# Kernel tuning notes

Measured on AMD Instinct MI355X. Metric: run time of the kernel, lower is better.

The kernel has to match this reference:

```python
import jax, jax.numpy as jnp
import numpy as np

NUM_CLASSES = 1000
NUM_NEIGHBOURS = 200
SIGMA = 10.0
GAUSS_CONST = 1.0 / (2.0 * SIGMA ** 2)


def setup_inputs() -> dict:
    key = jax.random.key(0)
    k1, k2, k3 = jax.random.split(key, 3)
    B, D, C = 512, 512, 100000
    features = jax.random.normal(k1, (B, D), dtype=jnp.float32)
    centres = jax.random.normal(k2, (C, D), dtype=jnp.float32)
    centre_labels = jax.random.randint(k3, (C,), 0, NUM_CLASSES)
    weight = jnp.zeros((C,), dtype=jnp.float32)
    return {"features": features, "centres": centres,
            "centre_labels": centre_labels, "weight": weight}


def _knn(features, centres, k):
    # squared euclidean distances [B, C] without materializing [B, C, D]
    f2 = jnp.sum(features * features, axis=1, keepdims=True)      # [B,1]
    c2 = jnp.sum(centres * centres, axis=1)                        # [C]
    d2 = f2 + c2[None, :] - 2.0 * features @ centres.T             # [B,C]
    _, idx = jax.lax.top_k(-d2, k)                                 # smallest k
    return idx                                                     # [B,k]


def reference(features, centres, centre_labels, weight):
    B = features.shape[0]
    K = NUM_NEIGHBOURS
    nbr = _knn(features, centres, K)                               # [B,K] int
    gathered = centres[nbr]                                        # [B,K,D]
    d2 = jnp.sum((features[:, None, :] - gathered) ** 2, axis=-1)  # [B,K]
    kernel_weights = jnp.exp(weight)                               # [C]
    d = jnp.exp(-d2 * GAUSS_CONST) * kernel_weights[nbr]           # [B,K]
    nbr_labels = centre_labels[nbr]                                # [B,K]
    rows = jnp.arange(B)[:, None]
    p = jnp.zeros((B, NUM_CLASSES), dtype=d.dtype).at[rows, nbr_labels].add(d)
    p = jnp.where(p == 0, 1e-10, p)
    p = p / jnp.sum(p, axis=1, keepdims=True)
    return jnp.log(p)
```

## Files before the change

### kernel.cpp

```cpp
#include <hip/hip_runtime.h>
#include <hip/hip_fp16.h>
#include <math.h>
#include <stdint.h>

#define D_DIM    512
#define NCLS     1000
#define KSEL     200
#define NBINS    1024
#define HREP     4
#define CAND_MAX 2048
#define GCONST   0.005
#define MARGIN   4.0f

typedef short s8v __attribute__((ext_vector_type(8)));
typedef float f4v __attribute__((ext_vector_type(4)));

#define GLOAD_LDS16(gp, lp) __builtin_amdgcn_global_load_lds( \
    (const __attribute__((address_space(1))) void*)(gp),      \
    (__attribute__((address_space(3))) void*)(lp), 16, 0, 0)

static __device__ __forceinline__ unsigned short f2bf(float x) {
    unsigned u = __float_as_uint(x);
    return (unsigned short)((u + 0x7FFFu + ((u >> 16) & 1u)) >> 16);
}

static __device__ __forceinline__ unsigned cvt_pk_bf16(float lo, float hi) {
    unsigned r;
    asm("v_cvt_pk_bf16_f32 %0, %1, %2" : "=v"(r) : "v"(lo), "v"(hi));
    return r;
}

__global__ __launch_bounds__(256)
void convertF(const float* __restrict__ F, unsigned short* __restrict__ Fb,
              float* __restrict__ f2)
{
    __shared__ float red[256];
    const int r = blockIdx.x, t = threadIdx.x;
    float2 v = *(const float2*)(F + (size_t)r * D_DIM + t * 2);
    ushort2 o; o.x = f2bf(v.x); o.y = f2bf(v.y);
    *(ushort2*)(Fb + (size_t)r * D_DIM + t * 2) = o;
    red[t] = v.x * v.x + v.y * v.y;
    __syncthreads();
    for (int off = 128; off > 0; off >>= 1) {
        if (t < off) red[t] += red[t + off];
        __syncthreads();
    }
    if (t == 0) f2[r] = red[0];
}

__global__ __launch_bounds__(512)
void mfma_gemm(const unsigned short* __restrict__ Fb,
               const float* __restrict__ C,
               const float* __restrict__ f2,
               __half* __restrict__ Dm, int N)
{
    __shared__ short smem[32 * 512 + 16 * 512];
    __shared__ float c2s[128];
    short* As = smem;
    short* Bs = smem + 32 * 512;
    const int t    = threadIdx.x;
    const int lane = t & 63;
    const int w    = t >> 6;
    const int wm   = w >> 1, wn = w & 1;
    const int m0   = blockIdx.x * 256;
    const int n0   = blockIdx.y * 128;
    const int lrow = lane >> 3;
    const int oct  = (lane & 7) ^ lrow;
    const int quad = lane >> 4;
    const int col  = lane & 15;

    f4v acc[4][4];
#pragma unroll
    for (int i = 0; i < 4; ++i)
#pragma unroll
        for (int j = 0; j < 4; ++j) acc[i][j] = (f4v){0.f, 0.f, 0.f, 0.f};

    float  c2part[2] = {0.f, 0.f};
    float4 ra[2], rb[2];

#pragma unroll
    for (int cc = 0; cc < 2; ++cc) {
        int row = (w * 2 + cc) * 8 + lrow;
        int rg  = n0 + row; rg = rg < N ? rg : N - 1;
        const float* gp = C + (size_t)rg * D_DIM + oct * 8;
        ra[cc] = *(const float4*)gp;
        rb[cc] = *(const float4*)(gp + 4);
    }

    for (int k0 = 0; k0 < D_DIM; k0 += 64) {
        __syncthreads();
#pragma unroll
        for (int cc = 0; cc < 4; ++cc) {
            int ch = w * 4 + cc;
            GLOAD_LDS16(Fb + (size_t)(m0 + ch * 8 + lrow) * D_DIM + k0 + oct * 8,
                        &As[ch * 512]);
        }
#pragma unroll
        for (int cc = 0; cc < 2; ++cc) {
            int row = (w * 2 + cc) * 8 + lrow;
            float4 va = ra[cc], vb = rb[cc];
            c2part[cc] += va.x*va.x + va.y*va.y + va.z*va.z + va.w*va.w
                        + vb.x*vb.x + vb.y*vb.y + vb.z*vb.z + vb.w*vb.w;
            uint4 o;
            o.x = cvt_pk_bf16(va.x, va.y);
            o.y = cvt_pk_bf16(va.z, va.w);
            o.z = cvt_pk_bf16(vb.x, vb.y);
            o.w = cvt_pk_bf16(vb.z, vb.w);
            *(uint4*)&Bs[row * 64 + (lane & 7) * 8] = o;
        }
        __syncthreads();

        if (k0 + 64 < D_DIM) {
#pragma unroll
            for (int cc = 0; cc < 2; ++cc) {
                int row = (w * 2 + cc) * 8 + lrow;
                int rg  = n0 + row; rg = rg < N ? rg : N - 1;
                const float* gp = C + (size_t)rg * D_DIM + (k0 + 64) + oct * 8;
                ra[cc] = *(const float4*)gp;
                rb[cc] = *(const float4*)(gp + 4);
            }
        }

#pragma unroll
        for (int kk = 0; kk < 2; ++kk) {
            int slot = (kk * 4 + quad) ^ (col & 7);
            s8v b[4];
#pragma unroll
            for (int j = 0; j < 4; ++j) {
                int row = wn * 64 + j * 16 + col;
                b[j] = *(s8v*)&Bs[row * 64 + slot * 8];
            }
#pragma unroll
            for (int i = 0; i < 4; ++i) {
                int row = wm * 64 + i * 16 + col;
                s8v a = *(s8v*)&As[row * 64 + slot * 8];
#pragma unroll
                for (int j = 0; j < 4; ++j)
                    acc[i][j] = __builtin_amdgcn_mfma_f32_16x16x32_bf16(
                        a, b[j], acc[i][j], 0, 0, 0);
            }
        }
    }

#pragma unroll
    for (int cc = 0; cc < 2; ++cc) {
        float s = c2part[cc];
        s += __shfl_xor(s, 1, 64);
        s += __shfl_xor(s, 2, 64);
        s += __shfl_xor(s, 4, 64);
        int row = (w * 2 + cc) * 8 + lrow;
        if ((lane & 7) == 0) c2s[row] = s;
    }
    __syncthreads();

    float c2v[4];
#pragma unroll
    for (int j = 0; j < 4; ++j)
        c2v[j] = c2s[wn * 64 + j * 16 + col];
    float fv[4][4];
#pragma unroll
    for (int i = 0; i < 4; ++i)
#pragma unroll
        for (int v = 0; v < 4; ++v)
            fv[i][v] = f2[m0 + wm * 64 + i * 16 + quad * 4 + v];

    __half* Cs = (__half*)smem;
#pragma unroll
    for (int h = 0; h < 2; ++h) {
        __syncthreads();
        if ((wm >> 1) == h) {
            int mlb = (wm & 1) * 64;
#pragma unroll
            for (int i = 0; i < 4; ++i) {
#pragma unroll
                for (int j = 0; j < 4; ++j) {
#pragma unroll
                    for (int v = 0; v < 4; ++v) {
                        int ml = mlb + i * 16 + quad * 4 + v;
                        int nl = wn * 64 + j * 16 + col;
                        float d2 = fv[i][v] + c2v[j] - 2.f * acc[i][j][v];
                        int slot = (nl >> 3) ^ (ml & 7);
                        Cs[ml * 128 + slot * 8 + (nl & 7)] = __float2half(d2);
                    }
                }
            }
        }
        __syncthreads();
#pragma unroll
        for (int it = 0; it < 4; ++it) {
            int idx = it * 512 + t;
            int row = idx >> 4;
            int o8  = idx & 15;
            int n   = n0 + o8 * 8;
            const __half* src = &Cs[row * 128 + ((o8 ^ (row & 7)) * 8)];
            __half* dst = Dm + (size_t)(m0 + h * 128 + row) * N + n;
            if (n + 7 < N) {
                *(uint4*)dst = *(const uint4*)src;
            } else if (n < N) {
                for (int e = 0; e < 8 && n + e < N; ++e) dst[e] = src[e];
            }
        }
    }
}

__global__ __launch_bounds__(1024)
void fused_select(const __half* __restrict__ Dm,
                  const float* __restrict__ F, const float* __restrict__ C,
                  const int* __restrict__ labels, const float* __restrict__ weight,
                  float* __restrict__ out, int N)
{
    __shared__ unsigned hist[NBINS * HREP];
    __shared__ float    fs[D_DIM];
    __shared__ int      idxs[CAND_MAX];
    __shared__ double   dists[CAND_MAX];
    __shared__ float    p[NCLS];
    __shared__ float    red[1024];
    __shared__ unsigned scanbuf[256];
    __shared__ float    sT;
    __shared__ unsigned scnt;

    const int r = blockIdx.x, t = threadIdx.x;
    for (int b = t; b < NBINS * HREP; b += 1024) hist[b] = 0u;
    for (int c = t; c < NCLS; c += 1024) p[c] = 0.f;
    for (int k = t; k < D_DIM; k += 1024) fs[k] = F[(size_t)r * D_DIM + k];
    if (t == 0) { sT = 1e30f; scnt = 0u; }
    __syncthreads();

    const __half* srow = Dm + (size_t)r * N;

    for (int j = t * 8; j < N; j += 8192) {
        uint4 sv = *(const uint4*)(srow + j);
        float2 s0 = __half22float2(*(__half2*)&sv.x);
        float2 s1 = __half22float2(*(__half2*)&sv.y);
        float2 s2 = __half22float2(*(__half2*)&sv.z);
        float2 s3 = __half22float2(*(__half2*)&sv.w);
        float d2v[8] = { s0.x, s0.y, s1.x, s1.y, s2.x, s2.y, s3.x, s3.y };
#pragma unroll
        for (int e = 0; e < 8; ++e) {
            int b = (int)(d2v[e] * 0.5f);
            b = b < 0 ? 0 : (b > NBINS - 1 ? NBINS - 1 : b);
            atomicAdd(&hist[(b << 2) + (t & 3)], 1u);
        }
    }
    __syncthreads();

    if (t < 256) {
        unsigned loc[NBINS / 256];
        unsigned s = 0;
#pragma unroll
        for (int i = 0; i < NBINS / 256; ++i) {
            int bb = t * (NBINS / 256) + i;
            loc[i] = hist[(bb << 2) + 0] + hist[(bb << 2) + 1]
                   + hist[(bb << 2) + 2] + hist[(bb << 2) + 3];
            s += loc[i];
        }
        scanbuf[t] = s;
        __syncthreads();
        unsigned pre = 0;
        for (int u = 0; u < t; ++u) pre += scanbuf[u];
        if (pre < KSEL && pre + s >= KSEL) {
            unsigned cum = pre;
            int b = NBINS - 1;
#pragma unroll
            for (int i = 0; i < NBINS / 256; ++i) {
                cum += loc[i];
                if (cum >= KSEL) { b = t * (NBINS / 256) + i; break; }
            }
            sT = 2.0f * (float)(b + 1) + MARGIN;
        }
    } else {
        __syncthreads();
    }
    __syncthreads();
    const float Tr = sT;

    for (int j = t * 8; j < N; j += 8192) {
        uint4 sv = *(const uint4*)(srow + j);
        float2 s0 = __half22float2(*(__half2*)&sv.x);
        float2 s1 = __half22float2(*(__half2*)&sv.y);
        float2 s2 = __half22float2(*(__half2*)&sv.z);
        float2 s3 = __half22float2(*(__half2*)&sv.w);
        float d2v[8] = { s0.x, s0.y, s1.x, s1.y, s2.x, s2.y, s3.x, s3.y };
#pragma unroll
        for (int e = 0; e < 8; ++e) {
            if (d2v[e] <= Tr) {
                unsigned pos = atomicAdd(&scnt, 1u);
                if (pos < CAND_MAX) idxs[pos] = j + e;
            }
        }
    }
    __syncthreads();
    int Nc = (int)scnt;
    if (Nc > CAND_MAX) Nc = CAND_MAX;

    {
        const int wv = t >> 6, lane = t & 63;
        for (int i = wv; i < Nc; i += 16) {
            int ci = idxs[i];
            const float* cp = C + (size_t)ci * D_DIM;
            float4 a  = *(const float4*)(cp + lane * 8);
            float4 b  = *(const float4*)(cp + lane * 8 + 4);
            float4 fa = *(const float4*)(fs + lane * 8);
            float4 fb = *(const float4*)(fs + lane * 8 + 4);
            double d0 = (double)fa.x - (double)a.x;
            double d1 = (double)fa.y - (double)a.y;
            double d2 = (double)fa.z - (double)a.z;
            double d3 = (double)fa.w - (double)a.w;
            double d4 = (double)fb.x - (double)b.x;
            double d5 = (double)fb.y - (double)b.y;
            double d6 = (double)fb.z - (double)b.z;
            double d7 = (double)fb.w - (double)b.w;
            double acc = d0*d0 + d1*d1 + d2*d2 + d3*d3
                       + d4*d4 + d5*d5 + d6*d6 + d7*d7;
#pragma unroll
            for (int off = 32; off > 0; off >>= 1)
                acc += __shfl_down(acc, off, 64);
            if (lane == 0) dists[i] = acc;
        }
    }
    __syncthreads();

    int ksel = KSEL < Nc ? KSEL : Nc;
    for (int i = t; i < Nc; i += 1024) {
        double di = dists[i];
        int    ii = idxs[i];
        int rank = 0;
        for (int j = 0; j < Nc; ++j) {
            double dj = dists[j];
            rank += (dj < di) || (dj == di && idxs[j] < ii);
        }
        if (rank < ksel) {
            double wgt = exp(-di * GCONST) * exp((double)weight[ii]);
            atomicAdd(&p[labels[ii]], (float)wgt);
        }
    }
    __syncthreads();

    float s = 0.f;
    for (int c = t; c < NCLS; c += 1024) {
        float v = p[c];
        if (v == 0.f) v = 1e-10f;
        p[c] = v;
        s += v;
    }
    red[t] = s;
    __syncthreads();
    for (int o = 512; o > 0; o >>= 1) {
        if (t < o) red[t] += red[t + o];
        __syncthreads();
    }
    float total = red[0];
    for (int c = t; c < NCLS; c += 1024)
        out[(size_t)r * NCLS + c] = logf(p[c] / total);
}

extern "C" void kernel_launch(void* const* d_in, const int* in_sizes, int n_in,
                              void* d_out, int out_size, void* d_ws, size_t ws_size,
                              hipStream_t stream)
{
    const float* features = (const float*)d_in[0];
    const float* centres  = (const float*)d_in[1];
    const int*   labels   = (const int*)d_in[2];
    const float* weight   = (const float*)d_in[3];
    const int B = in_sizes[0] / D_DIM;
    const int N = in_sizes[2];
    float* out = (float*)d_out;

    uint8_t* w = (uint8_t*)d_ws;
    size_t off = 0;
    auto alloc = [&](size_t bytes) -> uint8_t* {
        uint8_t* ptr = w + off;
        off = (off + bytes + 255) & ~(size_t)255;
        return ptr;
    };
    float*          f2 = (float*)alloc((size_t)B * 4);
    unsigned short* Fb = (unsigned short*)alloc((size_t)B * D_DIM * 2);
    __half*         Dm = (__half*)alloc((size_t)B * N * 2);
    (void)ws_size;

    convertF<<<B, 256, 0, stream>>>(features, Fb, f2);

    dim3 ggrid(B / 256, (N + 127) / 128);
    mfma_gemm<<<ggrid, 512, 0, stream>>>(Fb, centres, f2, Dm, N);

    fused_select<<<B, 1024, 0, stream>>>(Dm, features, centres,
                                         labels, weight, out, N);
}
```

Baseline: 464.2 us.

## Load A fragments directly from global and double-buffer B tile in LDS

Stops staging the bf16 feature tile (A) in shared memory and instead loads each wave's MFMA A fragments straight from global memory, relying on cache reuse. The LDS for the centre tile (B) is double-buffered, which cuts each k-step from two barriers to one. This trades LDS traffic and a barrier for extra global/L2 loads of A that sit in the MFMA critical path with no prefetch, so latency may be exposed.

Measured after the change: 495.6 us. 1.07x slower.

```diff
diff --git a/kernel.cpp b/kernel.cpp
--- a/kernel.cpp
+++ b/kernel.cpp
@@ -14,10 +14,6 @@
 
 typedef short s8v __attribute__((ext_vector_type(8)));
 typedef float f4v __attribute__((ext_vector_type(4)));
-
-#define GLOAD_LDS16(gp, lp) __builtin_amdgcn_global_load_lds( \
-    (const __attribute__((address_space(1))) void*)(gp),      \
-    (__attribute__((address_space(3))) void*)(lp), 16, 0, 0)
 
 static __device__ __forceinline__ unsigned short f2bf(float x) {
     unsigned u = __float_as_uint(x);
@@ -54,10 +50,8 @@
                const float* __restrict__ f2,
                __half* __restrict__ Dm, int N)
 {
-    __shared__ short smem[32 * 512 + 16 * 512];
+    __shared__ short smem[2 * 128 * 64];
     __shared__ float c2s[128];
-    short* As = smem;
-    short* Bs = smem + 32 * 512;
     const int t    = threadIdx.x;
     const int lane = t & 63;
     const int w    = t >> 6;
@@ -78,6 +72,11 @@
     float  c2part[2] = {0.f, 0.f};
     float4 ra[2], rb[2];
 
+    const unsigned short* Arow[4];
+#pragma unroll
+    for (int i = 0; i < 4; ++i)
+        Arow[i] = Fb + (size_t)(m0 + wm * 64 + i * 16 + col) * D_DIM + quad * 8;
+
 #pragma unroll
     for (int cc = 0; cc < 2; ++cc) {
         int row = (w * 2 + cc) * 8 + lrow;
@@ -87,14 +86,9 @@
         rb[cc] = *(const float4*)(gp + 4);
     }
 
-    for (int k0 = 0; k0 < D_DIM; k0 += 64) {
-        __syncthreads();
-#pragma unroll
-        for (int cc = 0; cc < 4; ++cc) {
-            int ch = w * 4 + cc;
-            GLOAD_LDS16(Fb + (size_t)(m0 + ch * 8 + lrow) * D_DIM + k0 + oct * 8,
-                        &As[ch * 512]);
-        }
+    int buf = 0;
+    for (int k0 = 0; k0 < D_DIM; k0 += 64, buf ^= 1) {
+        short* Bs = smem + buf * (128 * 64);
 #pragma unroll
         for (int cc = 0; cc < 2; ++cc) {
             int row = (w * 2 + cc) * 8 + lrow;
@@ -108,8 +102,6 @@
             o.w = cvt_pk_bf16(vb.z, vb.w);
             *(uint4*)&Bs[row * 64 + (lane & 7) * 8] = o;
         }
-        __syncthreads();
-
         if (k0 + 64 < D_DIM) {
 #pragma unroll
             for (int cc = 0; cc < 2; ++cc) {
@@ -120,6 +112,7 @@
                 rb[cc] = *(const float4*)(gp + 4);
             }
         }
+        __syncthreads();
 
 #pragma unroll
         for (int kk = 0; kk < 2; ++kk) {
@@ -130,15 +123,16 @@
                 int row = wn * 64 + j * 16 + col;
                 b[j] = *(s8v*)&Bs[row * 64 + slot * 8];
             }
-#pragma unroll
-            for (int i = 0; i < 4; ++i) {
-                int row = wm * 64 + i * 16 + col;
-                s8v a = *(s8v*)&As[row * 64 + slot * 8];
+            s8v a[4];
+#pragma unroll
+            for (int i = 0; i < 4; ++i)
+                a[i] = *(const s8v*)(Arow[i] + k0 + kk * 32);
+#pragma unroll
+            for (int i = 0; i < 4; ++i)
 #pragma unroll
                 for (int j = 0; j < 4; ++j)
                     acc[i][j] = __builtin_amdgcn_mfma_f32_16x16x32_bf16(
-                        a, b[j], acc[i][j], 0, 0, 0);
-            }
+                        a[i], b[j], acc[i][j], 0, 0, 0);
         }
     }
 
```

## Double-buffer A tile in LDS with async prefetch of next K slice

Applied to the files above, without the earlier changes.

The bf16 feature tile in LDS is now double-buffered, and the next K slice is issued through global_load_lds before the current slice's MFMAs run. Manual s_waitcnt vmcnt(8) plus raw s_barrier replace __syncthreads so the prefetched loads stay in flight across the barrier. The A fragments are also loaded into registers before the MFMA loop, and the c2 scratch now aliases the B buffer. The aim is to hide global-load latency behind compute, at the cost of more LDS per block and fragile hand-written wait counts that may lower occupancy.

Result: faster. 444.3 us (-4.3%).

```diff
diff --git a/kernel.cpp b/kernel.cpp
--- a/kernel.cpp
+++ b/kernel.cpp
@@ -54,10 +54,8 @@
                const float* __restrict__ f2,
                __half* __restrict__ Dm, int N)
 {
-    __shared__ short smem[32 * 512 + 16 * 512];
-    __shared__ float c2s[128];
-    short* As = smem;
-    short* Bs = smem + 32 * 512;
+    __shared__ short smem[2 * 256 * 64 + 128 * 64];
+    short* BsBase = smem + 2 * 256 * 64;
     const int t    = threadIdx.x;
     const int lane = t & 63;
     const int w    = t >> 6;
@@ -86,15 +84,19 @@
         ra[cc] = *(const float4*)gp;
         rb[cc] = *(const float4*)(gp + 4);
     }
-
-    for (int k0 = 0; k0 < D_DIM; k0 += 64) {
-        __syncthreads();
-#pragma unroll
-        for (int cc = 0; cc < 4; ++cc) {
-            int ch = w * 4 + cc;
-            GLOAD_LDS16(Fb + (size_t)(m0 + ch * 8 + lrow) * D_DIM + k0 + oct * 8,
-                        &As[ch * 512]);
-        }
+#pragma unroll
+    for (int cc = 0; cc < 4; ++cc) {
+        int ch = w * 4 + cc;
+        GLOAD_LDS16(Fb + (size_t)(m0 + ch * 8 + lrow) * D_DIM + 0 + oct * 8,
+                    &smem[ch * 512]);
+    }
+
+    int buf = 0;
+    for (int k0 = 0; k0 < D_DIM; k0 += 64, buf ^= 1) {
+        short* As  = smem + buf * (256 * 64);
+        short* Asn = smem + (buf ^ 1) * (256 * 64);
+        short* Bs  = BsBase;
+
 #pragma unroll
         for (int cc = 0; cc < 2; ++cc) {
             int row = (w * 2 + cc) * 8 + lrow;
@@ -108,7 +110,6 @@
             o.w = cvt_pk_bf16(vb.z, vb.w);
             *(uint4*)&Bs[row * 64 + (lane & 7) * 8] = o;
         }
-        __syncthreads();
 
         if (k0 + 64 < D_DIM) {
 #pragma unroll
@@ -119,7 +120,19 @@
                 ra[cc] = *(const float4*)gp;
                 rb[cc] = *(const float4*)(gp + 4);
             }
-        }
+#pragma unroll
+            for (int cc = 0; cc < 4; ++cc) {
+                int ch = w * 4 + cc;
+                GLOAD_LDS16(Fb + (size_t)(m0 + ch * 8 + lrow) * D_DIM
+                                + (k0 + 64) + oct * 8,
+                            &Asn[ch * 512]);
+            }
+            asm volatile("s_waitcnt vmcnt(8) lgkmcnt(0)" ::: "memory");
+        } else {
+            asm volatile("s_waitcnt vmcnt(0) lgkmcnt(0)" ::: "memory");
+        }
+        __builtin_amdgcn_s_barrier();
+        asm volatile("" ::: "memory");
 
 #pragma unroll
         for (int kk = 0; kk < 2; ++kk) {
@@ -130,18 +143,24 @@
                 int row = wn * 64 + j * 16 + col;
                 b[j] = *(s8v*)&Bs[row * 64 + slot * 8];
             }
+            s8v a[4];
 #pragma unroll
             for (int i = 0; i < 4; ++i) {
                 int row = wm * 64 + i * 16 + col;
-                s8v a = *(s8v*)&As[row * 64 + slot * 8];
+                a[i] = *(s8v*)&As[row * 64 + slot * 8];
+            }
+#pragma unroll
+            for (int i = 0; i < 4; ++i)
 #pragma unroll
                 for (int j = 0; j < 4; ++j)
                     acc[i][j] = __builtin_amdgcn_mfma_f32_16x16x32_bf16(
-                        a, b[j], acc[i][j], 0, 0, 0);
-            }
-        }
-    }
-
+                        a[i], b[j], acc[i][j], 0, 0, 0);
+        }
+        __builtin_amdgcn_s_barrier();
+        asm volatile("" ::: "memory");
+    }
+
+    float* c2s = (float*)BsBase;
 #pragma unroll
     for (int cc = 0; cc < 2; ++cc) {
         float s = c2part[cc];
```
